# Kernel optimization log

Hardware: AMD Instinct MI355X
Metric: run time of the kernel (lower is better)

## Reference

```python
import jax, jax.numpy as jnp
import numpy as np
from jax import lax

B, Cin, C, H, W, Ns, K = 2, 64, 64, 256, 1216, 20000, 9
HW = H * W
D = 2 * C + 3   # 131, MLP input dim
Dh = D // 2     # 65, MLP hidden dim


def _conv(x, w, b, relu):
    y = lax.conv_general_dilated(x, w, (1, 1), 'SAME',
                                 dimension_numbers=('NCHW', 'OIHW', 'NCHW'))
    y = y + b[None, :, None, None]
    return jax.nn.relu(y) if relu else y


def _mlp(f, w1, b1, w2, b2):
    # f: (B, Ns, K, D) -> (B, Ns, K, 1)
    h = jax.nn.leaky_relu(f @ w1 + b1, 0.2)
    return h @ w2 + b2


def setup_inputs() -> dict:
    ks = jax.random.split(jax.random.key(0), 32)
    s = 0.05
    rng = np.random.default_rng(0)
    # unique point indices per batch (torch scatter with dup indices is nondeterministic)
    pc = np.stack([np.sort(rng.choice(HW, Ns, replace=False)) for _ in range(B)])[:, None, :]
    inp = {
        'rgb': jax.random.normal(ks[0], (B, Cin, H, W), jnp.float32),
        'sdepth': jax.random.normal(ks[1], (B, Cin, H, W), jnp.float32),
        'pc_idx': jnp.asarray(pc, dtype=jnp.int32),
        'nbrs_idx': jax.random.randint(ks[2], (B, 1, Ns, K), 0, HW, dtype=jnp.int32),
        'nbrs_disp': jax.random.normal(ks[3], (B, 3, Ns, K), jnp.float32),
        'd_conv0_w': jax.random.normal(ks[4], (C, Cin, 3, 3), jnp.float32) * s,
        'd_conv0_b': jnp.zeros((C,), jnp.float32),
        'd_conv1_w': jax.random.normal(ks[5], (C, Cin, 3, 3), jnp.float32) * s,
        'd_conv1_b': jnp.zeros((C,), jnp.float32),
        'd_conv2_w': jax.random.normal(ks[6], (C, C, 3, 3), jnp.float32) * s,
        'd_conv2_b': jnp.zeros((C,), jnp.float32),
        'r_conv0_w': jax.random.normal(ks[7], (C, Cin, 3, 3), jnp.float32) * s,
        'r_conv0_b': jnp.zeros((C,), jnp.float32),
        'r_conv1_w': jax.random.normal(ks[8], (C, Cin, 3, 3), jnp.float32) * s,
        'r_conv1_b': jnp.zeros((C,), jnp.float32),
        'r_conv2_w': jax.random.normal(ks[9], (C, C, 3, 3), jnp.float32) * s,
        'r_conv2_b': jnp.zeros((C,), jnp.float32),
        'd_w1': jax.random.normal(ks[10], (D, Dh), jnp.float32) * s,
        'd_b1': jnp.zeros((Dh,), jnp.float32),
        'd_w2': jax.random.normal(ks[11], (Dh, 1), jnp.float32) * s,
        'd_b2': jnp.zeros((1,), jnp.float32),
        'r_w1': jax.random.normal(ks[12], (D, Dh), jnp.float32) * s,
        'r_b1': jnp.zeros((Dh,), jnp.float32),
        'r_w2': jax.random.normal(ks[13], (Dh, 1), jnp.float32) * s,
        'r_b2': jnp.zeros((1,), jnp.float32),
        'd_bias': jnp.zeros((C,), jnp.float32),
        'r_bias': jnp.zeros((C,), jnp.float32),
    }
    return inp


def reference(rgb, sdepth, pc_idx, nbrs_idx, nbrs_disp,
              d_conv0_w, d_conv0_b, d_conv1_w, d_conv1_b, d_conv2_w, d_conv2_b,
              r_conv0_w, r_conv0_b, r_conv1_w, r_conv1_b, r_conv2_w, r_conv2_b,
              d_w1, d_b1, d_w2, d_b2, r_w1, r_b1, r_w2, r_b2, d_bias, r_bias):
    d0 = _conv(sdepth, d_conv0_w, d_conv0_b, True)
    d1 = _conv(sdepth, d_conv1_w, d_conv1_b, False)
    r0 = _conv(rgb, r_conv0_w, r_conv0_b, True)
    r1 = _conv(rgb, r_conv1_w, r_conv1_b, False)

    d0f = d0.reshape(B, C, HW)
    r0f = r0.reshape(B, C, HW)

    pcb = jnp.broadcast_to(pc_idx, (B, C, Ns))
    nb = jnp.broadcast_to(nbrs_idx.reshape(B, 1, Ns * K), (B, C, Ns * K))
    d_s = jnp.take_along_axis(d0f, pcb, axis=2)                       # (B,C,Ns)
    d_nn = jnp.take_along_axis(d0f, nb, axis=2).reshape(B, C, Ns, K)  # (B,C,Ns,K)
    r_s = jnp.take_along_axis(r0f, pcb, axis=2)
    # NOTE: faithful to source, r neighbors are gathered from d_feat0
    r_nn = jnp.take_along_axis(d0f, nb, axis=2).reshape(B, C, Ns, K)

    feats = jnp.concatenate([d_nn - d_s[..., None],
                             r_nn - r_s[..., None],
                             nbrs_disp], axis=1)                      # (B,2C+3,Ns,K)
    feats = jnp.moveaxis(feats, 1, -1)                                # (B,Ns,K,2C+3)

    d_attn = jax.nn.softmax(_mlp(feats, d_w1, d_b1, d_w2, d_b2)[..., 0], axis=-1)  # (B,Ns,K)
    r_attn = jax.nn.softmax(_mlp(feats, r_w1, r_b1, r_w2, r_b2)[..., 0], axis=-1)

    d_feat = jnp.einsum('bnk,bcnk->bcn', d_attn, d_nn) + d_bias[None, :, None]
    r_feat = jnp.einsum('bnk,bcnk->bcn', r_attn, r_nn) + r_bias[None, :, None]

    scat = jax.vmap(lambda idx, src: jnp.zeros((C, HW), src.dtype).at[:, idx].set(src))
    d_new = scat(pc_idx[:, 0], d_feat)
    r_new = scat(pc_idx[:, 0], r_feat)

    # mask scatter in source uses index of shape (B,1,Ns): only channel 0 is set
    mask0 = jax.vmap(lambda i: jnp.zeros((HW,), d0f.dtype).at[i].set(1.0))(pc_idx[:, 0])
    masks = jnp.concatenate([mask0[:, None, :], jnp.zeros((B, C - 1, HW), d0f.dtype)], axis=1)

    d0f = (1.0 - masks) * d0f + d_new
    r0f = (1.0 - masks) * r0f + r_new

    d2 = _conv(d0f.reshape(B, C, H, W), d_conv2_w, d_conv2_b, False)
    r2 = _conv(r0f.reshape(B, C, H, W), r_conv2_w, r_conv2_b, False)
    return jax.nn.relu(d2 + d1), jax.nn.relu(r2 + r1)
```

## Files before the change

kernel.cpp:

```cpp
#include <hip/hip_runtime.h>

#define H_ 256
#define W_ 1216
#define HW_ (H_*W_)
#define B_ 2
#define Ns_ 20000
#define K_ 9
#define D_ 131
#define Dh_ 65

#define TPOS 66
#define CSTR (4*18*64*8)

typedef __attribute__((ext_vector_type(8))) short bf16x8;
typedef __attribute__((ext_vector_type(4))) float f32x4;

__device__ __forceinline__ float b2f(unsigned short u){
  union { unsigned int i; float f; } v; v.i = ((unsigned int)u) << 16; return v.f;
}
__device__ __forceinline__ unsigned short f2b(float f){
  union { float f; unsigned int i; } v; v.f = f;
  unsigned int r = (v.i + 0x7FFFu + ((v.i >> 16) & 1u)) >> 16;
  return (unsigned short)r;
}
__device__ __forceinline__ unsigned short f2h(float f){
  union { _Float16 h; unsigned short u; } v; v.h = (_Float16)f; return v.u;
}
__device__ __forceinline__ float h2f(unsigned short u){
  union { _Float16 h; unsigned short u; } v; v.u = u; return (float)v.h;
}
__device__ __forceinline__ void gld_lds16(const void* g, void* l){
  __builtin_amdgcn_global_load_lds(
      (const __attribute__((address_space(1))) unsigned int*)g,
      (__attribute__((address_space(3))) unsigned int*)l, 16, 0, 0);
}

struct WPtrs { const float* w[6]; };

__global__ void prep_w(WPtrs wp, unsigned short* __restrict__ Asw){
  int blk = blockIdx.x;
  int c = blk / 72, rem = blk % 72, mt = rem / 18, kc = rem % 18;
  int lane = threadIdx.x;
  const float* w = wp.w[c];
  int co = mt*16 + (lane & 15);
  int kb = kc*32 + (lane >> 4)*8;
  unsigned short* dst = Asw + ((size_t)blk*64 + lane)*8;
  #pragma unroll
  for (int j = 0; j < 8; ++j){
    int k = kb + j, tap = k >> 6, cin = k & 63;
    dst[j] = f2b(w[((size_t)co*64 + cin)*9 + tap]);
  }
}

__global__ void prep_wmlp(const float* __restrict__ dw1, const float* __restrict__ rw1,
                          unsigned short* __restrict__ Bm){
  int blk = blockIdx.x;
  int nt = blk / 5, ks = blk % 5;
  int lane = threadIdx.x;
  int col = nt*16 + (lane & 15);
  int kb  = ks*32 + (lane >> 4)*8;
  unsigned short* dst = Bm + ((size_t)blk*64 + lane)*8;
  #pragma unroll
  for (int jj = 0; jj < 8; ++jj){
    int row = kb + jj;
    float v = 0.f;
    if (row < D_ && col < 2*Dh_)
      v = (col < Dh_) ? dw1[(size_t)row*Dh_ + col] : rw1[(size_t)row*Dh_ + (col - Dh_)];
    dst[jj] = f2b(v);
  }
}

__global__ __launch_bounds__(256,4) void conv01_mfma(
    const float* __restrict__ xd, const float* __restrict__ xr,
    const unsigned short* __restrict__ Asw,
    const float* __restrict__ b0d, const float* __restrict__ b1d,
    const float* __restrict__ b0r, const float* __restrict__ b1r,
    unsigned short* __restrict__ d0t, unsigned short* __restrict__ u_d,
    unsigned short* __restrict__ r0t, unsigned short* __restrict__ u_r,
    unsigned short* __restrict__ y1h_d, unsigned short* __restrict__ y1h_r)
{
  __shared__ unsigned short tile[4*TPOS*64];
  int tid = threadIdx.x;
  int c0 = blockIdx.x*64, r0 = blockIdx.y*2;
  int t = blockIdx.z >> 1, b = blockIdx.z & 1;

  const float* x = t ? xr : xd;
  const unsigned short* Aswt = Asw + (size_t)(t ? 3 : 0)*CSTR;

  for (int e = tid; e < 4*TPOS*8; e += 256){
    int pos = e >> 3, slot = e & 7;
    int row = pos / TPOS, col = pos - row*TPOS;
    int gy = r0 - 1 + row, gx = c0 - 1 + col;
    int c8 = slot ^ (pos & 7);
    union { unsigned short us[8]; uint4 v; } pk;
    if (gy >= 0 && gy < H_ && gx >= 0 && gx < W_){
      const float* sp = x + ((size_t)b*64 + c8*8)*HW_ + (size_t)gy*W_ + gx;
      #pragma unroll
      for (int j = 0; j < 8; ++j) pk.us[j] = f2b(sp[(size_t)j*HW_]);
    } else {
      pk.v = (uint4){0u,0u,0u,0u};
    }
    *(uint4*)&tile[pos*64 + slot*8] = pk.v;
  }
  __syncthreads();

  int wave = tid >> 6, lane = tid & 63;
  int quad = lane >> 4, l15 = lane & 15;
  int cobase = (wave & 1)*32;
  int prow = wave >> 1;

  f32x4 acc[2][2][4];
  #pragma unroll
  for (int cv = 0; cv < 2; ++cv)
    #pragma unroll
    for (int mt = 0; mt < 2; ++mt)
      #pragma unroll
      for (int nt = 0; nt < 4; ++nt)
        acc[cv][mt][nt] = (f32x4){0.f,0.f,0.f,0.f};

  const unsigned short* Ap[2][2];
  #pragma unroll
  for (int cv = 0; cv < 2; ++cv)
    #pragma unroll
    for (int mt = 0; mt < 2; ++mt)
      Ap[cv][mt] = Aswt + ((size_t)((cv*4 + (wave&1)*2 + mt)*18)*64 + lane)*8;

  #pragma unroll
  for (int tap = 0; tap < 9; ++tap){
    int pbase = (prow + tap/3)*TPOS + l15 + (tap%3);
    int pk = pbase & 7;
    #pragma unroll
    for (int cc = 0; cc < 2; ++cc){
      int kc = tap*2 + cc;
      int sl = ((quad + 4*cc) ^ pk) << 3;
      bf16x8 a[2][2], bb[4];
      #pragma unroll
      for (int cv = 0; cv < 2; ++cv)
        #pragma unroll
        for (int mt = 0; mt < 2; ++mt)
          a[cv][mt] = *(const bf16x8*)(Ap[cv][mt] + (size_t)kc*512);
      #pragma unroll
      for (int nt = 0; nt < 4; ++nt)
        bb[nt] = *(const bf16x8*)&tile[(pbase + nt*16)*64 + sl];
      #pragma unroll
      for (int cv = 0; cv < 2; ++cv)
        #pragma unroll
        for (int mt = 0; mt < 2; ++mt)
          #pragma unroll
          for (int nt = 0; nt < 4; ++nt)
            acc[cv][mt][nt] = __builtin_amdgcn_mfma_f32_16x16x32_bf16(
                a[cv][mt], bb[nt], acc[cv][mt][nt], 0, 0, 0);
    }
  }

  unsigned short* y0t = t ? r0t : d0t;
  unsigned short* u   = t ? u_r  : u_d;
  unsigned short* y1h = t ? y1h_r : y1h_d;
  const float* b0 = t ? b0r : b0d;
  const float* b1 = t ? b1r : b1d;

  int gy = r0 + prow;
  #pragma unroll
  for (int mt = 0; mt < 2; ++mt){
    int co4 = cobase + mt*16 + quad*4;
    f32x4 bias0 = *(const f32x4*)&b0[co4];
    f32x4 bias1 = *(const f32x4*)&b1[co4];
    #pragma unroll
    for (int nt = 0; nt < 4; ++nt){
      int gx = c0 + nt*16 + l15;
      size_t gpix = (size_t)gy*W_ + gx;
      size_t toff = ((size_t)b*HW_ + gpix)*64 + co4;
      f32x4 v0 = acc[0][mt][nt] + bias0;
      ushort4 q;
      q.x = f2b(fmaxf(v0.x,0.f)); q.y = f2b(fmaxf(v0.y,0.f));
      q.z = f2b(fmaxf(v0.z,0.f)); q.w = f2b(fmaxf(v0.w,0.f));
      *(ushort4*)&y0t[toff] = q;
      *(ushort4*)&u[toff]   = q;
      f32x4 v1 = acc[1][mt][nt] + bias1;
      ushort4 h;
      h.x = f2h(v1.x); h.y = f2h(v1.y); h.z = f2h(v1.z); h.w = f2h(v1.w);
      *(ushort4*)&y1h[toff] = h;
    }
  }
}

__global__ __launch_bounds__(256,4) void conv2_mfma(
    const unsigned short* __restrict__ u_d, const unsigned short* __restrict__ u_r,
    const unsigned short* __restrict__ Asw,
    const float* __restrict__ biasd, const float* __restrict__ biasr,
    const unsigned short* __restrict__ y1h_d, const unsigned short* __restrict__ y1h_r,
    float* __restrict__ out)
{
  __shared__ unsigned short tile[4*TPOS*64];
  int tid = threadIdx.x;
  int c0 = blockIdx.x*64, r0 = blockIdx.y*2;
  int t = blockIdx.z >> 1, b = blockIdx.z & 1;

  const unsigned short* ut  = t ? u_r : u_d;
  const unsigned short* y1h = t ? y1h_r : y1h_d;
  const unsigned short* Aswt = Asw + (size_t)(t ? 5 : 2)*CSTR;
  const float* bias = t ? biasr : biasd;
  float* o = out + (size_t)t * B_ * 64 * HW_;

  {
    int wave = tid >> 6, lane = tid & 63;
    #pragma unroll 1
    for (int it = 0; it < 9; ++it){
      int e = wave*528 + it*64 + lane;
      bool active = (it < 8) || (lane < 16);
      if (active){
        int pos = e >> 3, slot = e & 7;
        int row = pos / TPOS, col = pos - row*TPOS;
        int gy = r0 - 1 + row, gx = c0 - 1 + col;
        int c8 = slot ^ (pos & 7);
        if (gy >= 0 && gy < H_ && gx >= 0 && gx < W_){
          const unsigned short* src = &ut[((size_t)b*HW_ + (size_t)gy*W_ + gx)*64 + c8*8];
          gld_lds16(src, &tile[(size_t)(wave*528 + it*64)*8]);
        } else {
          *(uint4*)&tile[(size_t)e*8] = (uint4){0u,0u,0u,0u};
        }
      }
    }
  }
  __syncthreads();

  int wave = tid >> 6, lane = tid & 63;
  int quad = lane >> 4, l15 = lane & 15;
  int cobase = (wave & 1)*32;
  int prow = wave >> 1;

  f32x4 acc[2][4];
  #pragma unroll
  for (int mt = 0; mt < 2; ++mt)
    #pragma unroll
    for (int nt = 0; nt < 4; ++nt)
      acc[mt][nt] = (f32x4){0.f,0.f,0.f,0.f};

  const unsigned short* Ap[2];
  #pragma unroll
  for (int mt = 0; mt < 2; ++mt)
    Ap[mt] = Aswt + ((size_t)(((wave&1)*2 + mt)*18)*64 + lane)*8;

  #pragma unroll
  for (int tap = 0; tap < 9; ++tap){
    int pbase = (prow + tap/3)*TPOS + l15 + (tap%3);
    int pk = pbase & 7;
    #pragma unroll
    for (int cc = 0; cc < 2; ++cc){
      int kc = tap*2 + cc;
      int sl = ((quad + 4*cc) ^ pk) << 3;
      bf16x8 a[2], bb[4];
      #pragma unroll
      for (int mt = 0; mt < 2; ++mt)
        a[mt] = *(const bf16x8*)(Ap[mt] + (size_t)kc*512);
      #pragma unroll
      for (int nt = 0; nt < 4; ++nt)
        bb[nt] = *(const bf16x8*)&tile[(pbase + nt*16)*64 + sl];
      #pragma unroll
      for (int mt = 0; mt < 2; ++mt)
        #pragma unroll
        for (int nt = 0; nt < 4; ++nt)
          acc[mt][nt] = __builtin_amdgcn_mfma_f32_16x16x32_bf16(
              a[mt], bb[nt], acc[mt][nt], 0, 0, 0);
    }
  }

  int gy = r0 + prow;
  #pragma unroll
  for (int mt = 0; mt < 2; ++mt){
    int co4 = cobase + mt*16 + quad*4;
    f32x4 bs = *(const f32x4*)&bias[co4];
    #pragma unroll
    for (int nt = 0; nt < 4; ++nt){
      int gx = c0 + nt*16 + l15;
      size_t gpix = (size_t)gy*W_ + gx;
      ushort4 h = *(const ushort4*)&y1h[((size_t)b*HW_ + gpix)*64 + co4];
      f32x4 v = acc[mt][nt] + bs;
      float r0v = v.x + h2f(h.x);
      float r1v = v.y + h2f(h.y);
      float r2v = v.z + h2f(h.z);
      float r3v = v.w + h2f(h.w);
      float* yo = o + ((size_t)b*64 + co4)*HW_ + gpix;
      yo[(size_t)0*HW_] = r0v > 0.f ? r0v : 0.f;
      yo[(size_t)1*HW_] = r1v > 0.f ? r1v : 0.f;
      yo[(size_t)2*HW_] = r2v > 0.f ? r2v : 0.f;
      yo[(size_t)3*HW_] = r3v > 0.f ? r3v : 0.f;
    }
  }
}

#define FBSTR 176
#define AW 4

struct __align__(16) WaveShm {
  unsigned short featsB[16][FBSTR];
  float feats[9][64];
  float ds[64], rs[64];
  float attnw[2][12];
};

__global__ __launch_bounds__(256) void attn_kernel(
    const unsigned short* __restrict__ d0t, const unsigned short* __restrict__ r0t,
    const int* __restrict__ pc_idx, const int* __restrict__ nbrs_idx,
    const float* __restrict__ disp,
    const unsigned short* __restrict__ Bmlp,
    const float* __restrict__ db2v, const float* __restrict__ dw2,
    const float* __restrict__ rb2v, const float* __restrict__ rw2,
    const float* __restrict__ dbias, const float* __restrict__ rbias,
    unsigned short* __restrict__ u_d, unsigned short* __restrict__ u_r)
{
  __shared__ WaveShm shm[AW];
  int tid = threadIdx.x;
  int wave = tid >> 6, lane = tid & 63;
  int quad = lane >> 4, l15 = lane & 15;
  int n = blockIdx.x * AW + wave;
  int b = blockIdx.y;
  WaveShm& S = shm[wave];

  int s = pc_idx[(size_t)b*Ns_ + n];
  s = __builtin_amdgcn_readfirstlane(s);

  int myidx = (lane < 9) ? nbrs_idx[((size_t)b*Ns_ + n)*K_ + lane] : 0;
  int idx8 = __shfl(myidx, 8);

  {
    uint4 z = {0u,0u,0u,0u};
    unsigned short* fb = &S.featsB[0][0];
    #pragma unroll
    for (int it = 0; it < 6; ++it){
      int e = it*64 + lane;
      if (e < 16*FBSTR/8) *(uint4*)&fb[e*8] = z;
    }
  }
  if (lane < 27){
    int m = lane / 9, k = lane - m*9;
    S.featsB[k][128 + m] = f2b(disp[(((size_t)b*3 + m)*Ns_ + n)*K_ + k]);
  }

  int grow = lane >> 3, gp = lane & 7;
  int gidx = __shfl(myidx, grow);
  uint4 g1 = *(const uint4*)&d0t[((size_t)b*HW_ + (size_t)gidx)*64 + gp*8];
  uint4 g2 = {0u,0u,0u,0u};
  if (lane < 24){
    int r2 = 8 + grow;
    int idx2 = (r2 == 8) ? idx8 : s;
    const unsigned short* base = (r2 == 10) ? r0t : d0t;
    g2 = *(const uint4*)&base[((size_t)b*HW_ + (size_t)idx2)*64 + gp*8];
  }

  float dn[8];
  {
    const unsigned short* us = (const unsigned short*)&g1;
    #pragma unroll
    for (int j = 0; j < 8; ++j){ dn[j] = b2f(us[j]); S.feats[grow][gp*8 + j] = dn[j]; }
  }
  if (lane >= 8 && lane < 24){
    const unsigned short* us = (const unsigned short*)&g2;
    float* dst = (lane < 16) ? &S.ds[(lane - 8)*8] : &S.rs[(lane - 16)*8];
    #pragma unroll
    for (int j = 0; j < 8; ++j) dst[j] = b2f(us[j]);
  }

  {
    unsigned short od[8], orr[8];
    #pragma unroll
    for (int j = 0; j < 8; ++j){
      int c = gp*8 + j;
      od[j]  = f2b(dn[j] - S.ds[c]);
      orr[j] = f2b(dn[j] - S.rs[c]);
    }
    *(uint4*)&S.featsB[grow][gp*8]      = *(uint4*)od;
    *(uint4*)&S.featsB[grow][64 + gp*8] = *(uint4*)orr;
  }
  if (lane < 8){
    const unsigned short* us = (const unsigned short*)&g2;
    unsigned short od[8], orr[8];
    #pragma unroll
    for (int j = 0; j < 8; ++j){
      int c = lane*8 + j;
      float v = b2f(us[j]);
      S.feats[8][c] = v;
      od[j]  = f2b(v - S.ds[c]);
      orr[j] = f2b(v - S.rs[c]);
    }
    *(uint4*)&S.featsB[8][lane*8]      = *(uint4*)od;
    *(uint4*)&S.featsB[8][64 + lane*8] = *(uint4*)orr;
  }

  bf16x8 afr[5];
  #pragma unroll
  for (int ks = 0; ks < 5; ++ks)
    afr[ks] = *(const bf16x8*)&S.featsB[l15][ks*32 + quad*8];

  float pd[2][4];
  #pragma unroll
  for (int m = 0; m < 2; ++m)
    #pragma unroll
    for (int r = 0; r < 4; ++r) pd[m][r] = 0.f;

  #pragma unroll
  for (int nt = 0; nt < 9; ++nt){
    f32x4 acc = (f32x4){0.f,0.f,0.f,0.f};
    const unsigned short* bp = Bmlp + ((size_t)nt*5*64 + lane)*8;
    #pragma unroll
    for (int ks = 0; ks < 5; ++ks){
      bf16x8 bfr = *(const bf16x8*)(bp + (size_t)ks*512);
      acc = __builtin_amdgcn_mfma_f32_16x16x32_bf16(afr[ks], bfr, acc, 0, 0, 0);
    }
    int jq = nt*16 + l15;
    if (jq < 2*Dh_){
      int mlp = (jq >= Dh_) ? 1 : 0;
      int j = jq - mlp*Dh_;
      float w2 = mlp ? rw2[j] : dw2[j];
      #pragma unroll
      for (int r = 0; r < 4; ++r){
        float h = acc[r];
        h = h > 0.f ? h : 0.2f*h;
        pd[mlp][r] += h * w2;
      }
    }
  }

  #pragma unroll
  for (int mask = 1; mask <= 8; mask <<= 1)
    #pragma unroll
    for (int m = 0; m < 2; ++m)
      #pragma unroll
      for (int r = 0; r < 4; ++r)
        pd[m][r] += __shfl_xor(pd[m][r], mask);

  float b2c[2] = { db2v[0], rb2v[0] };
  #pragma unroll
  for (int m = 0; m < 2; ++m){
    float lg[4];
    float mx = -3.4e38f;
    #pragma unroll
    for (int r = 0; r < 4; ++r){
      lg[r] = pd[m][r] + b2c[m];
      if (quad*4 + r < 9) mx = fmaxf(mx, lg[r]);
    }
    mx = fmaxf(mx, __shfl_xor(mx, 16));
    mx = fmaxf(mx, __shfl_xor(mx, 32));
    float ex[4], sum = 0.f;
    #pragma unroll
    for (int r = 0; r < 4; ++r){
      int k = quad*4 + r;
      ex[r] = (k < 9) ? __expf(lg[r] - mx) : 0.f;
      sum += ex[r];
    }
    sum += __shfl_xor(sum, 16);
    sum += __shfl_xor(sum, 32);
    float inv = 1.f / sum;
    if (l15 == 0){
      #pragma unroll
      for (int r = 0; r < 4; ++r){
        int k = quad*4 + r;
        if (k < 9) S.attnw[m][k] = ex[r] * inv;
      }
    }
  }

  {
    int c = lane;
    #pragma unroll
    for (int m = 0; m < 2; ++m){
      float f = (m ? rbias : dbias)[c];
      #pragma unroll
      for (int k = 0; k < 9; ++k)
        f += S.attnw[m][k] * S.feats[k][c];
      float base = (c == 0) ? 0.f : (m ? S.rs[c] : S.ds[c]);
      unsigned short* u = m ? u_r : u_d;
      u[((size_t)b*HW_ + (size_t)s)*64 + c] = f2b(base + f);
    }
  }
}

extern "C" void kernel_launch(void* const* d_in, const int* in_sizes, int n_in,
                              void* d_out, int out_size, void* d_ws, size_t ws_size,
                              hipStream_t stream)
{
  (void)in_sizes; (void)n_in; (void)out_size; (void)ws_size;

  const float* rgb       = (const float*)d_in[0];
  const float* sdepth    = (const float*)d_in[1];
  const int*   pc_idx    = (const int*)d_in[2];
  const int*   nbrs_idx  = (const int*)d_in[3];
  const float* nbrs_disp = (const float*)d_in[4];

  WPtrs wp;
  wp.w[0] = (const float*)d_in[5];
  wp.w[1] = (const float*)d_in[7];
  wp.w[2] = (const float*)d_in[9];
  wp.w[3] = (const float*)d_in[11];
  wp.w[4] = (const float*)d_in[13];
  wp.w[5] = (const float*)d_in[15];
  const float* d_conv0_b = (const float*)d_in[6];
  const float* d_conv1_b = (const float*)d_in[8];
  const float* d_conv2_b = (const float*)d_in[10];
  const float* r_conv0_b = (const float*)d_in[12];
  const float* r_conv1_b = (const float*)d_in[14];
  const float* r_conv2_b = (const float*)d_in[16];
  const float* d_w1 = (const float*)d_in[17];
  const float* d_w2 = (const float*)d_in[19];
  const float* d_b2 = (const float*)d_in[20];
  const float* r_w1 = (const float*)d_in[21];
  const float* r_w2 = (const float*)d_in[23];
  const float* r_b2 = (const float*)d_in[24];
  const float* d_bias = (const float*)d_in[25];
  const float* r_bias = (const float*)d_in[26];

  char* ws = (char*)d_ws;
  const size_t TSZ = (size_t)B_ * HW_ * 64 * 2;
  unsigned short* u_d   = (unsigned short*)(ws + 0*TSZ);
  unsigned short* u_r   = (unsigned short*)(ws + 1*TSZ);
  unsigned short* d0t   = (unsigned short*)(ws + 2*TSZ);
  unsigned short* r0t   = (unsigned short*)(ws + 3*TSZ);
  unsigned short* y1h_d = (unsigned short*)(ws + 4*TSZ);
  unsigned short* y1h_r = (unsigned short*)(ws + 5*TSZ);
  unsigned short* Asw   = (unsigned short*)(ws + 6*TSZ);
  unsigned short* Bmlp  = Asw + 6*CSTR;

  prep_w<<<432, 64, 0, stream>>>(wp, Asw);
  prep_wmlp<<<45, 64, 0, stream>>>(d_w1, r_w1, Bmlp);

  float* out = (float*)d_out;

  dim3 cgrid(W_/64, H_/2, 4);

  conv01_mfma<<<cgrid, 256, 0, stream>>>(sdepth, rgb, Asw,
      d_conv0_b, d_conv1_b, r_conv0_b, r_conv1_b,
      d0t, u_d, r0t, u_r, y1h_d, y1h_r);

  attn_kernel<<<dim3(Ns_/AW, B_), 256, 0, stream>>>(
      d0t, r0t, pc_idx, nbrs_idx, nbrs_disp,
      Bmlp,
      d_b2, d_w2, r_b2, r_w2,
      d_bias, r_bias,
      u_d, u_r);

  conv2_mfma<<<cgrid, 256, 0, stream>>>(u_d, u_r, Asw,
      d_conv2_b, r_conv2_b, y1h_d, y1h_r, out);
}
```

Before: 1.260 ms.

## Drop duplicate conv0 output copy via compact attention buffer and scatter; enlarge conv tiles

conv01 no longer writes a second copy (d0t/r0t) of the conv0 output. Instead, attention reads neighbours from u_d/u_r directly, writes its results to a compact per-point buffer, and a new scatter kernel copies them into u_d/u_r before conv2. Both conv kernels also move from 2 to 4 output rows per block with 512 threads, which cuts halo reloads. The cost is one extra small kernel launch and larger per-block LDS use, which may lower occupancy.

```diff
diff --git a/kernel.cpp b/kernel.cpp
--- a/kernel.cpp
+++ b/kernel.cpp
@@ -11,6 +11,7 @@
 
 #define TPOS 66
 #define CSTR (4*18*64*8)
+#define ROWS 4
 
 typedef __attribute__((ext_vector_type(8))) short bf16x8;
 typedef __attribute__((ext_vector_type(4))) float f32x4;
@@ -70,24 +71,23 @@
   }
 }
 
-__global__ __launch_bounds__(256,4) void conv01_mfma(
+__global__ __launch_bounds__(512,4) void conv01_mfma(
     const float* __restrict__ xd, const float* __restrict__ xr,
     const unsigned short* __restrict__ Asw,
     const float* __restrict__ b0d, const float* __restrict__ b1d,
     const float* __restrict__ b0r, const float* __restrict__ b1r,
-    unsigned short* __restrict__ d0t, unsigned short* __restrict__ u_d,
-    unsigned short* __restrict__ r0t, unsigned short* __restrict__ u_r,
+    unsigned short* __restrict__ u_d, unsigned short* __restrict__ u_r,
     unsigned short* __restrict__ y1h_d, unsigned short* __restrict__ y1h_r)
 {
-  __shared__ unsigned short tile[4*TPOS*64];
+  __shared__ unsigned short tile[(ROWS+2)*TPOS*64];
   int tid = threadIdx.x;
-  int c0 = blockIdx.x*64, r0 = blockIdx.y*2;
+  int c0 = blockIdx.x*64, r0 = blockIdx.y*ROWS;
   int t = blockIdx.z >> 1, b = blockIdx.z & 1;
 
   const float* x = t ? xr : xd;
   const unsigned short* Aswt = Asw + (size_t)(t ? 3 : 0)*CSTR;
 
-  for (int e = tid; e < 4*TPOS*8; e += 256){
+  for (int e = tid; e < (ROWS+2)*TPOS*8; e += 512){
     int pos = e >> 3, slot = e & 7;
     int row = pos / TPOS, col = pos - row*TPOS;
     int gy = r0 - 1 + row, gx = c0 - 1 + col;
@@ -153,8 +153,7 @@
     }
   }
 
-  unsigned short* y0t = t ? r0t : d0t;
-  unsigned short* u   = t ? u_r  : u_d;
+  unsigned short* u   = t ? u_r   : u_d;
   unsigned short* y1h = t ? y1h_r : y1h_d;
   const float* b0 = t ? b0r : b0d;
   const float* b1 = t ? b1r : b1d;
@@ -174,8 +173,7 @@
       ushort4 q;
       q.x = f2b(fmaxf(v0.x,0.f)); q.y = f2b(fmaxf(v0.y,0.f));
       q.z = f2b(fmaxf(v0.z,0.f)); q.w = f2b(fmaxf(v0.w,0.f));
-      *(ushort4*)&y0t[toff] = q;
-      *(ushort4*)&u[toff]   = q;
+      *(ushort4*)&u[toff] = q;
       f32x4 v1 = acc[1][mt][nt] + bias1;
       ushort4 h;
       h.x = f2h(v1.x); h.y = f2h(v1.y); h.z = f2h(v1.z); h.w = f2h(v1.w);
@@ -184,16 +182,19 @@
   }
 }
 
-__global__ __launch_bounds__(256,4) void conv2_mfma(
+#define C2ELEM ((ROWS+2)*TPOS*8)
+#define C2PW   (C2ELEM/8)
+
+__global__ __launch_bounds__(512,4) void conv2_mfma(
     const unsigned short* __restrict__ u_d, const unsigned short* __restrict__ u_r,
     const unsigned short* __restrict__ Asw,
     const float* __restrict__ biasd, const float* __restrict__ biasr,
     const unsigned short* __restrict__ y1h_d, const unsigned short* __restrict__ y1h_r,
     float* __restrict__ out)
 {
-  __shared__ unsigned short tile[4*TPOS*64];
+  __shared__ unsigned short tile[(ROWS+2)*TPOS*64];
   int tid = threadIdx.x;
-  int c0 = blockIdx.x*64, r0 = blockIdx.y*2;
+  int c0 = blockIdx.x*64, r0 = blockIdx.y*ROWS;
   int t = blockIdx.z >> 1, b = blockIdx.z & 1;
 
   const unsigned short* ut  = t ? u_r : u_d;
@@ -202,20 +203,20 @@
   const float* bias = t ? biasr : biasd;
   float* o = out + (size_t)t * B_ * 64 * HW_;
 
+  int wave = tid >> 6, lane = tid & 63;
   {
-    int wave = tid >> 6, lane = tid & 63;
     #pragma unroll 1
-    for (int it = 0; it < 9; ++it){
-      int e = wave*528 + it*64 + lane;
-      bool active = (it < 8) || (lane < 16);
-      if (active){
+    for (int it = 0; it < 7; ++it){
+      int off = it*64 + lane;
+      if (off < C2PW){
+        int e = wave*C2PW + off;
         int pos = e >> 3, slot = e & 7;
         int row = pos / TPOS, col = pos - row*TPOS;
         int gy = r0 - 1 + row, gx = c0 - 1 + col;
         int c8 = slot ^ (pos & 7);
         if (gy >= 0 && gy < H_ && gx >= 0 && gx < W_){
           const unsigned short* src = &ut[((size_t)b*HW_ + (size_t)gy*W_ + gx)*64 + c8*8];
-          gld_lds16(src, &tile[(size_t)(wave*528 + it*64)*8]);
+          gld_lds16(src, &tile[(size_t)(wave*C2PW + it*64)*8]);
         } else {
           *(uint4*)&tile[(size_t)e*8] = (uint4){0u,0u,0u,0u};
         }
@@ -224,7 +225,6 @@
   }
   __syncthreads();
 
-  int wave = tid >> 6, lane = tid & 63;
   int quad = lane >> 4, l15 = lane & 15;
   int cobase = (wave & 1)*32;
   int prow = wave >> 1;
@@ -300,14 +300,14 @@
 };
 
 __global__ __launch_bounds__(256) void attn_kernel(
-    const unsigned short* __restrict__ d0t, const unsigned short* __restrict__ r0t,
+    const unsigned short* __restrict__ u_d, const unsigned short* __restrict__ u_r,
     const int* __restrict__ pc_idx, const int* __restrict__ nbrs_idx,
     const float* __restrict__ disp,
     const unsigned short* __restrict__ Bmlp,
     const float* __restrict__ db2v, const float* __restrict__ dw2,
     const float* __restrict__ rb2v, const float* __restrict__ rw2,
     const float* __restrict__ dbias, const float* __restrict__ rbias,
-    unsigned short* __restrict__ u_d, unsigned short* __restrict__ u_r)
+    unsigned short* __restrict__ cd, unsigned short* __restrict__ cr)
 {
   __shared__ WaveShm shm[AW];
   int tid = threadIdx.x;
@@ -339,12 +339,12 @@
 
   int grow = lane >> 3, gp = lane & 7;
   int gidx = __shfl(myidx, grow);
-  uint4 g1 = *(const uint4*)&d0t[((size_t)b*HW_ + (size_t)gidx)*64 + gp*8];
+  uint4 g1 = *(const uint4*)&u_d[((size_t)b*HW_ + (size_t)gidx)*64 + gp*8];
   uint4 g2 = {0u,0u,0u,0u};
   if (lane < 24){
     int r2 = 8 + grow;
     int idx2 = (r2 == 8) ? idx8 : s;
-    const unsigned short* base = (r2 == 10) ? r0t : d0t;
+    const unsigned short* base = (r2 == 10) ? u_r : u_d;
     g2 = *(const uint4*)&base[((size_t)b*HW_ + (size_t)idx2)*64 + gp*8];
   }
 
@@ -469,10 +469,25 @@
       for (int k = 0; k < 9; ++k)
         f += S.attnw[m][k] * S.feats[k][c];
       float base = (c == 0) ? 0.f : (m ? S.rs[c] : S.ds[c]);
-      unsigned short* u = m ? u_r : u_d;
-      u[((size_t)b*HW_ + (size_t)s)*64 + c] = f2b(base + f);
-    }
-  }
+      unsigned short* cc_ = m ? cr : cd;
+      cc_[((size_t)b*Ns_ + (size_t)n)*64 + c] = f2b(base + f);
+    }
+  }
+}
+
+__global__ __launch_bounds__(256) void scatter_k(
+    const unsigned short* __restrict__ cd, const unsigned short* __restrict__ cr,
+    const int* __restrict__ pc_idx,
+    unsigned short* __restrict__ u_d, unsigned short* __restrict__ u_r)
+{
+  int gid = blockIdx.x*256 + threadIdx.x;
+  int p = gid >> 3, q = gid & 7;
+  int n = p % Ns_, b = p / Ns_;
+  int s = pc_idx[(size_t)b*Ns_ + n];
+  size_t so = ((size_t)b*HW_ + (size_t)s)*64 + q*8;
+  size_t co = ((size_t)b*Ns_ + (size_t)n)*64 + q*8;
+  *(uint4*)&u_d[so] = *(const uint4*)&cd[co];
+  *(uint4*)&u_r[so] = *(const uint4*)&cr[co];
 }
 
 extern "C" void kernel_launch(void* const* d_in, const int* in_sizes, int n_in,
@@ -511,13 +526,14 @@
 
   char* ws = (char*)d_ws;
   const size_t TSZ = (size_t)B_ * HW_ * 64 * 2;
+  const size_t CSZ = (size_t)B_ * Ns_ * 64 * 2;
   unsigned short* u_d   = (unsigned short*)(ws + 0*TSZ);
   unsigned short* u_r   = (unsigned short*)(ws + 1*TSZ);
-  unsigned short* d0t   = (unsigned short*)(ws + 2*TSZ);
-  unsigned short* r0t   = (unsigned short*)(ws + 3*TSZ);
-  unsigned short* y1h_d = (unsigned short*)(ws + 4*TSZ);
-  unsigned short* y1h_r = (unsigned short*)(ws + 5*TSZ);
-  unsigned short* Asw   = (unsigned short*)(ws + 6*TSZ);
+  unsigned short* y1h_d = (unsigned short*)(ws + 2*TSZ);
+  unsigned short* y1h_r = (unsigned short*)(ws + 3*TSZ);
+  unsigned short* cd    = (unsigned short*)(ws + 4*TSZ);
+  unsigned short* cr    = (unsigned short*)(ws + 4*TSZ + CSZ);
+  unsigned short* Asw   = (unsigned short*)(ws + 4*TSZ + 2*CSZ);
   unsigned short* Bmlp  = Asw + 6*CSTR;
 
   prep_w<<<432, 64, 0, stream>>>(wp, Asw);
@@ -525,19 +541,21 @@
 
   float* out = (float*)d_out;
 
-  dim3 cgrid(W_/64, H_/2, 4);
-
-  conv01_mfma<<<cgrid, 256, 0, stream>>>(sdepth, rgb, Asw,
+  dim3 cgrid(W_/64, H_/ROWS, 4);
+
+  conv01_mfma<<<cgrid, 512, 0, stream>>>(sdepth, rgb, Asw,
       d_conv0_b, d_conv1_b, r_conv0_b, r_conv1_b,
-      d0t, u_d, r0t, u_r, y1h_d, y1h_r);
+      u_d, u_r, y1h_d, y1h_r);
 
   attn_kernel<<<dim3(Ns_/AW, B_), 256, 0, stream>>>(
-      d0t, r0t, pc_idx, nbrs_idx, nbrs_disp,
+      u_d, u_r, pc_idx, nbrs_idx, nbrs_disp,
       Bmlp,
       d_b2, d_w2, r_b2, r_w2,
       d_bias, r_bias,
-      u_d, u_r);
-
-  conv2_mfma<<<cgrid, 256, 0, stream>>>(u_d, u_r, Asw,
+      cd, cr);
+
+  scatter_k<<<(B_*Ns_*8)/256, 256, 0, stream>>>(cd, cr, pc_idx, u_d, u_r);
+
+  conv2_mfma<<<cgrid, 512, 0, stream>>>(u_d, u_r, Asw,
       d_conv2_b, r_conv2_b, y1h_d, y1h_r, out);
 }
```

After: 1.142 ms. 1.1x faster.
